# Kernel optimization log

Hardware: AMD Instinct MI355X
Metric: run time of the kernel (lower is better)

## Reference

```python
import jax, jax.numpy as jnp
import numpy as np

L_SEG = 20   # number of CFT segments (hard-coded in original forward)
M_CHEB = 8   # Chebyshev quadrature order per segment


def _cft_magnitude(x, modes):
    """|CFT(x)| at integer frequencies [0, modes).

    Faithful to vectorized_batched_cft_decomposed with L=20, M=8, but only
    evaluated at the first `modes` frequencies (identical values; the original
    computes all rfft freqs then slices). Segment loop is folded into a single
    einsum by absorbing the per-segment phase shift into the quadrature weights.
    x: (B, C, N) real. Returns (B, C, modes) float.
    """
    n = x.shape[-1]
    t = jnp.linspace(0.0, 1.0, n)
    freqs = jnp.arange(modes, dtype=x.dtype)  # rfftfreq(n, d=1/n)[:modes]
    seg_len = 1.0 / L_SEG
    starts = jnp.linspace(0.0, 1.0, L_SEG + 1)[:-1]  # (L,)
    k = jnp.arange(M_CHEB, dtype=x.dtype)
    cheb = -jnp.cos((2.0 * k + 1.0) * jnp.pi / (2.0 * M_CHEB))  # (M,) nodes in [-1,1]
    T = jnp.cos(k[:, None] * jnp.arccos(cheb)[None, :])  # (K=M, M) Chebyshev T_k at nodes
    angle = cheb[:, None] * (freqs[None, :] * (2.0 * jnp.pi * seg_len / 2.0))  # (M, F)
    Wr = jnp.einsum('km,mf->kf', T, jnp.cos(angle)) * (seg_len / 2.0)  # (M, F)
    Wi = jnp.einsum('km,mf->kf', T, -jnp.sin(angle)) * (seg_len / 2.0)
    # piecewise-linear interpolation of x at the Chebyshev nodes of every segment
    t_seg = starts[:, None] + seg_len / 2.0 * (cheb + 1.0)[None, :]  # (L, M)
    right = jnp.clip(jnp.searchsorted(t, t_seg), 0, n - 1)
    left = jnp.clip(right - 1, 0, None)
    t_l, t_r = t[left], t[right]
    denom = jnp.where(t_r - t_l == 0.0, 1.0, t_r - t_l)
    w_r = (t_seg - t_l) / denom
    w_l = 1.0 - w_r
    seg = w_l * x[:, :, left] + w_r * x[:, :, right]  # (B, C, L, M)
    # per-segment phase shift exp(-i*2*pi*f*a) folded into combined weights
    phi = 2.0 * jnp.pi * starts[:, None] * freqs[None, :]  # (L, F)
    cs, sn = jnp.cos(phi), jnp.sin(phi)
    Ar = Wr[None] * cs[:, None, :] + Wi[None] * sn[:, None, :]   # (L, M, F)
    Ai = -Wr[None] * sn[:, None, :] + Wi[None] * cs[:, None, :]
    real = jnp.einsum('bclm,lmf->bcf', seg, Ar)
    imag = jnp.einsum('bclm,lmf->bcf', seg, Ai)
    return jnp.sqrt(real * real + imag * imag)


def setup_inputs() -> dict:
    key = jax.random.key(0)
    ks = jax.random.split(key, 4)
    B, Cin, Cout, N, modes = 32, 64, 64, 8192, 32
    scale = 1.0 / (Cin * Cout)
    return {
        'x': jax.random.normal(ks[0], (B, Cin, N), dtype=jnp.float32),
        'w1_real': scale * jax.random.uniform(ks[1], (Cin, Cout, modes), dtype=jnp.float32),
        'w1_imag': scale * jax.random.uniform(ks[2], (Cin, Cout, modes), dtype=jnp.float32),
        'gate_w': jax.random.normal(ks[3], (Cout, Cin), dtype=jnp.float32) / np.sqrt(Cin),
        'ln_gamma': jnp.ones((modes,), dtype=jnp.float32),
        'ln_beta': jnp.zeros((modes,), dtype=jnp.float32),
    }


def reference(x, w1_real, w1_imag, gate_w, ln_gamma, ln_beta):
    n = x.shape[-1]
    n_rfft = n // 2 + 1
    modes = w1_real.shape[-1]
    x_fft = jnp.fft.rfft(x)  # (B, C, n_rfft) complex64
    # CFT magnitude is detached in the original (x_cft.detach())
    mag = jax.lax.stop_gradient(_cft_magnitude(x, modes))  # (B, C, modes)
    # LayerNorm over the modes axis (eps = 1e-5, torch default)
    mu = jnp.mean(mag, axis=-1, keepdims=True)
    var = jnp.mean((mag - mu) ** 2, axis=-1, keepdims=True)
    g_norm = (mag - mu) / jnp.sqrt(var + 1e-5) * ln_gamma + ln_beta
    # 1x1 conv (no bias) over channels, then sigmoid gate
    gate = jax.nn.sigmoid(jnp.einsum('oi,bif->bof', gate_w, g_norm))  # (B, Cout, modes)
    gated = x_fft[:, :, :modes] * gate  # requires Cin == Cout
    w1 = w1_real + 1j * w1_imag  # (Cin, Cout, modes) complex
    out_modes = jnp.einsum('bix,iox->box', gated, w1)
    pad = jnp.zeros(out_modes.shape[:2] + (n_rfft - modes,), dtype=out_modes.dtype)
    out_ft = jnp.concatenate([out_modes, pad], axis=-1)
    return jnp.fft.irfft(out_ft, n=n)
```

## Files before the change

### kernel.cpp

```cpp
#include <hip/hip_runtime.h>
#include <hip/hip_bf16.h>
#include <math.h>

#define NN    8192
#define NROWS 2048
#define FF    32
#define LM    160

static constexpr int TRIG   = 0;
static constexpr int W1RT   = 524288;
static constexpr int W1IT   = 655360;
static constexpr int GWT    = 786432;
static constexpr int AR_    = 790528;
static constexpr int AI_    = 795648;
static constexpr int WL_    = 800768;
static constexpr int WR_    = 800928;
static constexpr int IL_    = 801088;
static constexpr int IR_    = 801248;
static constexpr int XR_    = 801408;
static constexpr int XI_    = 866944;
static constexpr int GN_    = 932480;
static constexpr int ARAI   = 998016;
static constexpr int TRIGT_ = 1129088;

#define PI_D 3.14159265358979323846

__global__ __launch_bounds__(256) void k_trig(float* __restrict__ ws) {
  int idx = blockIdx.x * 256 + threadIdx.x;
  int k4 = idx >> 8, f = (idx >> 2) & 63, j = idx & 3;
  int n = 4 * k4 + j;
  int fr = f & 31;
  int p = (fr * n) & (NN - 1);
  float ang = (float)p * (float)(2.0 * PI_D / (double)NN);
  float s, c;
  sincosf(ang, &s, &c);
  float v = (f < 32) ? c : s;
  ws[TRIG + idx] = v;
  ws[TRIGT_ + f * NN + n] = v;
}

__global__ __launch_bounds__(256) void k_cft_tables(float* __restrict__ ws) {
  int tid = blockIdx.x * 256 + threadIdx.x;
  if (tid >= LM * FF) return;
  int j = tid >> 5, f = tid & 31;
  int l = j >> 3, m = j & 7;
  const double cheb[8] = {
    -0.98078528040323044913, -0.83146961230254523708,
    -0.55557023301960222474, -0.19509032201612826785,
     0.19509032201612826785,  0.55557023301960222474,
     0.83146961230254523708,  0.98078528040323044913 };

  double Wr = 0.0, Wi = 0.0;
  #pragma unroll
  for (int mm = 0; mm < 8; ++mm) {
    double c = cheb[mm];
    double T;
    if (m == 0) T = 1.0;
    else {
      double a = 1.0, b = c;
      for (int q = 1; q < m; ++q) { double t = 2.0 * c * b - a; a = b; b = t; }
      T = b;
    }
    double ang = c * (double)f * (PI_D * 0.05);
    Wr += T * cos(ang);
    Wi += T * (-sin(ang));
  }
  Wr *= 0.025; Wi *= 0.025;
  double phi = 2.0 * PI_D * ((double)l * 0.05) * (double)f;
  double cs = cos(phi), sn = sin(phi);
  ws[AR_ + j * FF + f] = (float)(Wr * cs + Wi * sn);
  ws[AI_ + j * FF + f] = (float)(-Wr * sn + Wi * cs);

  if (f == 0) {
    double v = (double)l * 0.05 + 0.025 * (cheb[m] + 1.0);
    int r = (int)(v * 8191.0);
    while ((double)r / 8191.0 < v) ++r;
    while (r > 0 && (double)(r - 1) / 8191.0 >= v) --r;
    if (r > 8191) r = 8191;
    int le = r - 1; if (le < 0) le = 0;
    double tl = (double)le / 8191.0, tr = (double)r / 8191.0;
    double den = (tr - tl == 0.0) ? 1.0 : (tr - tl);
    double wr = (v - tl) / den;
    ws[WL_ + j] = (float)(1.0 - wr);
    ws[WR_ + j] = (float)wr;
    ((int*)ws)[IL_ + j] = le;
    ((int*)ws)[IR_ + j] = r;
  }
}

__global__ __launch_bounds__(256) void k_transpose(const float* __restrict__ w1r,
                                                   const float* __restrict__ w1i,
                                                   const float* __restrict__ gw,
                                                   float* __restrict__ ws) {
  int idx = blockIdx.x * 256 + threadIdx.x;
  if (idx >= 32 * 64 * 64) return;
  int o = idx & 63, i = (idx >> 6) & 63, f = idx >> 12;
  ws[W1RT + (f * 64 + i) * 64 + o] = w1r[(i * 64 + o) * FF + f];
  ws[W1IT + (f * 64 + i) * 64 + o] = w1i[(i * 64 + o) * FF + f];
  if (idx < 4096) {
    ws[GWT + idx] = gw[(idx & 63) * 64 + (idx >> 6)];
  }
}

__global__ __launch_bounds__(256, 4) void k_fwd_gemm(const float* __restrict__ x,
                                                     const float* __restrict__ ws,
                                                     float* __restrict__ part) {
  __shared__ __align__(16) float xs[64 * 128];
  const int rt = blockIdx.x >> 6, kc = blockIdx.x & 63;
  const int t = threadIdx.x;
  const int w = t >> 6, lane = t & 63;
  const int half = lane >> 5, fl = lane & 31;
  const int rblock = rt * 64;
  const float4* __restrict__ tg4 = (const float4*)(ws + TRIG);
  const int k40 = kc * 32;

  const int c4 = t & 31, r0 = t >> 5;
  const int kb = kc * 128;
  #pragma unroll
  for (int p = 0; p < 8; ++p) {
    int row = r0 + 8 * p;
    float4 v = *(const float4*)(x + (size_t)(rblock + row) * NN + kb + c4 * 4);
    *(float4*)(&xs[row * 128 + c4 * 4]) = v;
  }

  float accC[8], accS[8];
  #pragma unroll
  for (int r = 0; r < 8; ++r) { accC[r] = 0.f; accS[r] = 0.f; }

  __syncthreads();

  const float* __restrict__ xbase = &xs[(w * 16 + half * 8) * 128];

#define FWD_LOAD(DST, COL)                                                      \
  {                                                                             \
    _Pragma("unroll")                                                           \
    for (int j = 0; j < 8; ++j)                                                 \
      DST[j] = *(const float4*)(xbase + j * 128 + (COL) * 4);                   \
  }

#define FWD_FMA(XV, TC, TS)                                                     \
  {                                                                             \
    _Pragma("unroll")                                                           \
    for (int j = 0; j < 8; ++j) {                                               \
      accC[j] = fmaf(XV[j].w, (TC).w, fmaf(XV[j].z, (TC).z,                     \
                fmaf(XV[j].y, (TC).y, fmaf(XV[j].x, (TC).x, accC[j]))));        \
      accS[j] = fmaf(XV[j].w, (TS).w, fmaf(XV[j].z, (TS).z,                     \
                fmaf(XV[j].y, (TS).y, fmaf(XV[j].x, (TS).x, accS[j]))));        \
    }                                                                           \
  }

  float4 xva[8], xvb[8];
  float4 tc = tg4[(size_t)k40 * 64 + fl];
  float4 tn = tg4[(size_t)k40 * 64 + 32 + fl];
  FWD_LOAD(xva, 0);

  for (int it = 0; it < 30; it += 2) {
    float4 tcB = tg4[(size_t)(k40 + it + 1) * 64 + fl];
    float4 tnB = tg4[(size_t)(k40 + it + 1) * 64 + 32 + fl];
    FWD_LOAD(xvb, it + 1);
    FWD_FMA(xva, tc, tn);
    float4 tcA = tg4[(size_t)(k40 + it + 2) * 64 + fl];
    float4 tnA = tg4[(size_t)(k40 + it + 2) * 64 + 32 + fl];
    FWD_LOAD(xva, it + 2);
    FWD_FMA(xvb, tcB, tnB);
    tc = tcA; tn = tnA;
  }
  float4 tcL = tg4[(size_t)(k40 + 31) * 64 + fl];
  float4 tnL = tg4[(size_t)(k40 + 31) * 64 + 32 + fl];
  FWD_LOAD(xvb, 31);
  FWD_FMA(xva, tc, tn);
  FWD_FMA(xvb, tcL, tnL);
#undef FWD_LOAD
#undef FWD_FMA

  float* __restrict__ pp = part + ((size_t)kc * NROWS + rblock + w * 16 + half * 8) * 64;
  #pragma unroll
  for (int j = 0; j < 8; ++j) {
    pp[j * 64 + fl]      = accC[j];
    pp[j * 64 + 32 + fl] = accS[j];
  }
}

__global__ __launch_bounds__(256) void k_fred(const float* __restrict__ part,
                                              float* __restrict__ ws) {
  int idx = blockIdx.x * 256 + threadIdx.x;
  int row = idx >> 4, fq = idx & 15;
  const float4* __restrict__ p4 = (const float4*)part;
  float4 s = make_float4(0.f, 0.f, 0.f, 0.f);
  #pragma unroll 16
  for (int kc = 0; kc < 64; ++kc) {
    float4 v = p4[((size_t)kc * NROWS + row) * 16 + fq];
    s.x += v.x; s.y += v.y; s.z += v.z; s.w += v.w;
  }
  if (fq < 8) {
    *(float4*)(ws + XR_ + row * FF + fq * 4) = s;
  } else {
    float4 n = make_float4(-s.x, -s.y, -s.z, -s.w);
    *(float4*)(ws + XI_ + row * FF + (fq - 8) * 4) = n;
  }
}

__global__ __launch_bounds__(256) void k_cft(const float* __restrict__ x,
                                             const float* __restrict__ gamma,
                                             const float* __restrict__ beta,
                                             float* __restrict__ ws) {
  const int sub = threadIdx.x >> 6, li = threadIdx.x & 63;
  const int row = blockIdx.x * 4 + sub;
  const float* __restrict__ xr = x + (size_t)row * NN;
  __shared__ float seg[4][LM];
  #pragma unroll
  for (int g = 0; g < 3; ++g) {
    int j = li + 64 * g;
    if (j < LM) {
      int il = ((const int*)ws)[IL_ + j];
      int ir = ((const int*)ws)[IR_ + j];
      seg[sub][j] = ws[WL_ + j] * xr[il] + ws[WR_ + j] * xr[ir];
    }
  }
  __syncthreads();
  if (li < FF) {
    float re = 0.f, im = 0.f;
    #pragma unroll 8
    for (int j = 0; j < LM; ++j) {
      float sv = seg[sub][j];
      re = fmaf(sv, ws[AR_ + j * FF + li], re);
      im = fmaf(sv, ws[AI_ + j * FF + li], im);
    }
    float mag = sqrtf(re * re + im * im);
    float mu = mag;
    mu += __shfl_xor(mu, 1);  mu += __shfl_xor(mu, 2);  mu += __shfl_xor(mu, 4);
    mu += __shfl_xor(mu, 8);  mu += __shfl_xor(mu, 16);
    mu *= (1.0f / 32.0f);
    float d = mag - mu;
    float vv = d * d;
    vv += __shfl_xor(vv, 1);  vv += __shfl_xor(vv, 2);  vv += __shfl_xor(vv, 4);
    vv += __shfl_xor(vv, 8);  vv += __shfl_xor(vv, 16);
    vv *= (1.0f / 32.0f);
    float g = d / sqrtf(vv + 1e-5f) * gamma[li] + beta[li];
    ws[GN_ + row * FF + li] = g;
  }
}

__global__ __launch_bounds__(64) void k_gate(float* __restrict__ ws) {
  int bidx = blockIdx.x;
  int b = bidx >> 5, f = bidx & 31;
  int o = threadIdx.x;
  __shared__ float gn[64], gr[64], gi[64];
  int rowb = b * 64;
  gn[o] = ws[GN_ + (rowb + o) * FF + f];
  float xre = ws[XR_ + (rowb + o) * FF + f];
  float xim = ws[XI_ + (rowb + o) * FF + f];
  __syncthreads();
  float acc = 0.f;
  #pragma unroll 16
  for (int i = 0; i < 64; ++i)
    acc = fmaf(ws[GWT + i * 64 + o], gn[i], acc);
  float gate = 1.0f / (1.0f + expf(-acc));
  gr[o] = xre * gate;
  gi[o] = xim * gate;
  __syncthreads();
  float Yr = 0.f, Yi = 0.f;
  const float* __restrict__ w1rt = ws + W1RT + f * 4096;
  const float* __restrict__ w1it = ws + W1IT + f * 4096;
  #pragma unroll 8
  for (int i = 0; i < 64; ++i) {
    float a = gr[i], bb2 = gi[i];
    float wr = w1rt[i * 64 + o], wi = w1it[i * 64 + o];
    Yr = fmaf(a, wr, Yr); Yr = fmaf(-bb2, wi, Yr);
    Yi = fmaf(a, wi, Yi); Yi = fmaf(bb2, wr, Yi);
  }
  float* A = ws + ARAI + (size_t)(rowb + o) * 64;
  if (f == 0) {
    A[0]  = Yr * (1.0f / (float)NN);
    A[32] = 0.0f;
  } else {
    A[f]      = Yr * (2.0f / (float)NN);
    A[32 + f] = -Yi * (2.0f / (float)NN);
  }
}

__global__ __launch_bounds__(256) void k_inv(const float* __restrict__ ws,
                                             float* __restrict__ out) {
  __shared__ __align__(16) float As[32 * 64];
  const int blk = blockIdx.x;
  const int bb = blk >> 5, cc = blk & 31;
  const int t = threadIdx.x;
  const int w = t >> 6, lane = t & 63;
  const int rowbase = bb * 32;
  const float* __restrict__ trigt = ws + TRIGT_;
  const int colb = cc * 256 + lane * 4;

  float4 tg0 = *(const float4*)(trigt + (size_t)0 * NN + colb);
  float4 tg1 = *(const float4*)(trigt + (size_t)1 * NN + colb);
  float4 tg2 = *(const float4*)(trigt + (size_t)2 * NN + colb);
  float4 tg3 = *(const float4*)(trigt + (size_t)3 * NN + colb);

  #pragma unroll
  for (int p = 0; p < 2; ++p) {
    int idx = t + 256 * p;
    int r = idx >> 4, q = idx & 15;
    *(float4*)(&As[r * 64 + q * 4]) =
        *(const float4*)(ws + ARAI + (size_t)(rowbase + r) * 64 + q * 4);
  }

  float4 acc[8];
  #pragma unroll
  for (int r = 0; r < 8; ++r) acc[r] = make_float4(0.f, 0.f, 0.f, 0.f);

  __syncthreads();

#define INV_STEP(F0)                                                            \
  {                                                                             \
    _Pragma("unroll")                                                           \
    for (int r = 0; r < 8; ++r) {                                               \
      float4 av = *(const float4*)(&As[(w * 8 + r) * 64 + (F0)]);               \
      acc[r].x = fmaf(av.x, tg0.x, acc[r].x); acc[r].y = fmaf(av.x, tg0.y, acc[r].y); \
      acc[r].z = fmaf(av.x, tg0.z, acc[r].z); acc[r].w = fmaf(av.x, tg0.w, acc[r].w); \
      acc[r].x = fmaf(av.y, tg1.x, acc[r].x); acc[r].y = fmaf(av.y, tg1.y, acc[r].y); \
      acc[r].z = fmaf(av.y, tg1.z, acc[r].z); acc[r].w = fmaf(av.y, tg1.w, acc[r].w); \
      acc[r].x = fmaf(av.z, tg2.x, acc[r].x); acc[r].y = fmaf(av.z, tg2.y, acc[r].y); \
      acc[r].z = fmaf(av.z, tg2.z, acc[r].z); acc[r].w = fmaf(av.z, tg2.w, acc[r].w); \
      acc[r].x = fmaf(av.w, tg3.x, acc[r].x); acc[r].y = fmaf(av.w, tg3.y, acc[r].y); \
      acc[r].z = fmaf(av.w, tg3.z, acc[r].z); acc[r].w = fmaf(av.w, tg3.w, acc[r].w); \
    }                                                                           \
  }

  for (int fo = 0; fo < 15; ++fo) {
    int f0 = fo * 4;
    float4 n0 = *(const float4*)(trigt + (size_t)(f0 + 4) * NN + colb);
    float4 n1 = *(const float4*)(trigt + (size_t)(f0 + 5) * NN + colb);
    float4 n2 = *(const float4*)(trigt + (size_t)(f0 + 6) * NN + colb);
    float4 n3 = *(const float4*)(trigt + (size_t)(f0 + 7) * NN + colb);
    INV_STEP(f0);
    tg0 = n0; tg1 = n1; tg2 = n2; tg3 = n3;
  }
  INV_STEP(60);
#undef INV_STEP

  #pragma unroll
  for (int r = 0; r < 8; ++r) {
    int row = rowbase + w * 8 + r;
    *(float4*)(out + (size_t)row * NN + colb) = acc[r];
  }
}

extern "C" void kernel_launch(void* const* d_in, const int* in_sizes, int n_in,
                              void* d_out, int out_size, void* d_ws, size_t ws_size,
                              hipStream_t stream) {
  const float* x     = (const float*)d_in[0];
  const float* w1r   = (const float*)d_in[1];
  const float* w1i   = (const float*)d_in[2];
  const float* gw    = (const float*)d_in[3];
  const float* gamma = (const float*)d_in[4];
  const float* beta  = (const float*)d_in[5];
  float* out = (float*)d_out;
  float* ws = (float*)d_ws;
  float* part = (float*)d_out;

  hipLaunchKernelGGL(k_trig,       dim3(2048), dim3(256), 0, stream, ws);
  hipLaunchKernelGGL(k_cft_tables, dim3(20),   dim3(256), 0, stream, ws);
  hipLaunchKernelGGL(k_transpose,  dim3(512),  dim3(256), 0, stream, w1r, w1i, gw, ws);
  hipLaunchKernelGGL(k_fwd_gemm,   dim3(2048), dim3(256), 0, stream, x, ws, part);
  hipLaunchKernelGGL(k_fred,       dim3(128),  dim3(256), 0, stream, part, ws);
  hipLaunchKernelGGL(k_cft,        dim3(512),  dim3(256), 0, stream, x, gamma, beta, ws);
  hipLaunchKernelGGL(k_gate,       dim3(1024), dim3(64),  0, stream, ws);
  hipLaunchKernelGGL(k_inv,        dim3(2048), dim3(256), 0, stream, ws, out);
}
```

Measured before the change: 212.2 us.

## Stage x and trig tiles into LDS via direct global-to-LDS loads

The forward DFT GEMM kernel now uses the global_load_lds builtin to copy both the x tile and this block's trig-table slice straight into shared memory, bypassing registers. The inner loop then reads the trig values from LDS instead of global memory, and the hand-written double-buffered register pipeline is replaced by a simple unrolled loop. This is meant to cut global trig-table traffic and register pressure. In exchange it doubles LDS use per block (32KB more), drops the occupancy hint from launch_bounds, and gives up explicit load/compute overlap.

```diff
diff --git a/kernel.cpp b/kernel.cpp
--- a/kernel.cpp
+++ b/kernel.cpp
@@ -25,6 +25,12 @@
 
 #define PI_D 3.14159265358979323846
 
+__device__ __forceinline__ void load_lds16(const float* g, float* l) {
+  __builtin_amdgcn_global_load_lds(
+      (const __attribute__((address_space(1))) void*)g,
+      (__attribute__((address_space(3))) void*)l, 16, 0, 0);
+}
+
 __global__ __launch_bounds__(256) void k_trig(float* __restrict__ ws) {
   int idx = blockIdx.x * 256 + threadIdx.x;
   int k4 = idx >> 8, f = (idx >> 2) & 63, j = idx & 3;
@@ -102,25 +108,30 @@
   }
 }
 
-__global__ __launch_bounds__(256, 4) void k_fwd_gemm(const float* __restrict__ x,
-                                                     const float* __restrict__ ws,
-                                                     float* __restrict__ part) {
+__global__ __launch_bounds__(256) void k_fwd_gemm(const float* __restrict__ x,
+                                                  const float* __restrict__ ws,
+                                                  float* __restrict__ part) {
   __shared__ __align__(16) float xs[64 * 128];
+  __shared__ __align__(16) float ts[32 * 256];
   const int rt = blockIdx.x >> 6, kc = blockIdx.x & 63;
   const int t = threadIdx.x;
   const int w = t >> 6, lane = t & 63;
   const int half = lane >> 5, fl = lane & 31;
   const int rblock = rt * 64;
-  const float4* __restrict__ tg4 = (const float4*)(ws + TRIG);
-  const int k40 = kc * 32;
-
+  const int kb = kc * 128;
   const int c4 = t & 31, r0 = t >> 5;
-  const int kb = kc * 128;
+
   #pragma unroll
   for (int p = 0; p < 8; ++p) {
     int row = r0 + 8 * p;
-    float4 v = *(const float4*)(x + (size_t)(rblock + row) * NN + kb + c4 * 4);
-    *(float4*)(&xs[row * 128 + c4 * 4]) = v;
+    load_lds16(x + (size_t)(rblock + row) * NN + kb + c4 * 4,
+               &xs[row * 128 + c4 * 4]);
+  }
+  const float* __restrict__ tsrc = ws + TRIG + (size_t)kc * 8192;
+  #pragma unroll
+  for (int p = 0; p < 8; ++p) {
+    int q = 256 * p + t;
+    load_lds16(tsrc + q * 4, &ts[q * 4]);
   }
 
   float accC[8], accS[8];
@@ -129,49 +140,22 @@
 
   __syncthreads();
 
-  const float* __restrict__ xbase = &xs[(w * 16 + half * 8) * 128];
-
-#define FWD_LOAD(DST, COL)                                                      \
-  {                                                                             \
-    _Pragma("unroll")                                                           \
-    for (int j = 0; j < 8; ++j)                                                 \
-      DST[j] = *(const float4*)(xbase + j * 128 + (COL) * 4);                   \
-  }
-
-#define FWD_FMA(XV, TC, TS)                                                     \
-  {                                                                             \
-    _Pragma("unroll")                                                           \
-    for (int j = 0; j < 8; ++j) {                                               \
-      accC[j] = fmaf(XV[j].w, (TC).w, fmaf(XV[j].z, (TC).z,                     \
-                fmaf(XV[j].y, (TC).y, fmaf(XV[j].x, (TC).x, accC[j]))));        \
-      accS[j] = fmaf(XV[j].w, (TS).w, fmaf(XV[j].z, (TS).z,                     \
-                fmaf(XV[j].y, (TS).y, fmaf(XV[j].x, (TS).x, accS[j]))));        \
-    }                                                                           \
-  }
-
-  float4 xva[8], xvb[8];
-  float4 tc = tg4[(size_t)k40 * 64 + fl];
-  float4 tn = tg4[(size_t)k40 * 64 + 32 + fl];
-  FWD_LOAD(xva, 0);
-
-  for (int it = 0; it < 30; it += 2) {
-    float4 tcB = tg4[(size_t)(k40 + it + 1) * 64 + fl];
-    float4 tnB = tg4[(size_t)(k40 + it + 1) * 64 + 32 + fl];
-    FWD_LOAD(xvb, it + 1);
-    FWD_FMA(xva, tc, tn);
-    float4 tcA = tg4[(size_t)(k40 + it + 2) * 64 + fl];
-    float4 tnA = tg4[(size_t)(k40 + it + 2) * 64 + 32 + fl];
-    FWD_LOAD(xva, it + 2);
-    FWD_FMA(xvb, tcB, tnB);
-    tc = tcA; tn = tnA;
-  }
-  float4 tcL = tg4[(size_t)(k40 + 31) * 64 + fl];
-  float4 tnL = tg4[(size_t)(k40 + 31) * 64 + 32 + fl];
-  FWD_LOAD(xvb, 31);
-  FWD_FMA(xva, tc, tn);
-  FWD_FMA(xvb, tcL, tnL);
-#undef FWD_LOAD
-#undef FWD_FMA
+  const float* __restrict__ xb = &xs[(w * 16 + half * 8) * 128];
+  const float* __restrict__ tb = &ts[fl * 4];
+
+  #pragma unroll 8
+  for (int it = 0; it < 32; ++it) {
+    float4 tc = *(const float4*)(tb + it * 256);
+    float4 tn = *(const float4*)(tb + it * 256 + 128);
+    #pragma unroll
+    for (int j = 0; j < 8; ++j) {
+      float4 xv = *(const float4*)(xb + j * 128 + it * 4);
+      accC[j] = fmaf(xv.w, tc.w, fmaf(xv.z, tc.z,
+                fmaf(xv.y, tc.y, fmaf(xv.x, tc.x, accC[j]))));
+      accS[j] = fmaf(xv.w, tn.w, fmaf(xv.z, tn.z,
+                fmaf(xv.y, tn.y, fmaf(xv.x, tn.x, accS[j]))));
+    }
+  }
 
   float* __restrict__ pp = part + ((size_t)kc * NROWS + rblock + w * 16 + half * 8) * 64;
   #pragma unroll
```

New measurement: 214.9 us. About the same (+1.3%).
